# Optimization experiments

Measured on AMD Instinct MI355X. Metric: run time of the kernel, lower is better.

The kernel has to match this reference:

```python
import jax, jax.numpy as jnp
import numpy as np

B, T, F = 2048, 60, 89
H = 1024
OUT = 30  # output_predicted_chords


def setup_inputs() -> dict:
    key = jax.random.key(0)
    k1, k2, k3, k4 = jax.random.split(key, 4)
    # small init scale keeps the relu-activated recurrence numerically stable
    s = 0.02
    return {
        "x": jax.random.normal(k1, (B, T, F), dtype=jnp.float32),
        "W": jax.random.normal(k2, (F, 4 * H), dtype=jnp.float32) * s,
        "U": jax.random.normal(k3, (H, 4 * H), dtype=jnp.float32) * s,
        "b": jnp.zeros((4 * H,), dtype=jnp.float32),
        "Wd": jax.random.normal(k4, (H, OUT), dtype=jnp.float32) * s,
        "bd": jnp.zeros((OUT,), dtype=jnp.float32),
    }


def _lstm_last_h(x, W, U, b):
    """Keras LSTM(activation='relu', recurrent_activation='sigmoid').
    Gate order in Keras kernels: i, f, c (candidate), o.
    Returns last hidden state h_T of shape [B, H]."""
    Bsz = x.shape[0]
    Hdim = U.shape[0]
    # precompute input projections for all timesteps: [T, B, 4H]
    xz = jnp.einsum('btf,fg->tbg', x, W) + b

    def step(carry, xz_t):
        h, c = carry
        z = xz_t + h @ U                      # [B, 4H]
        i, f, g, o = jnp.split(z, 4, axis=-1)
        i = jax.nn.sigmoid(i)
        f = jax.nn.sigmoid(f)
        g = jax.nn.relu(g)                    # activation='relu' on candidate
        o = jax.nn.sigmoid(o)
        c = f * c + i * g
        h = o * jax.nn.relu(c)                # activation='relu' on cell output
        return (h, c), None

    h0 = jnp.zeros((Bsz, Hdim), dtype=x.dtype)
    c0 = jnp.zeros((Bsz, Hdim), dtype=x.dtype)
    (hT, _), _ = jax.lax.scan(step, (h0, c0), xz)
    return hT


def reference(x, W, U, b, Wd, bd):
    # LSTM(return_sequences=True) then take x[:, -1, :] == last hidden state
    hT = _lstm_last_h(x, W, U, b)             # [B, H]
    y = hT @ Wd + bd                           # [B, OUT]
    return y.reshape(-1, OUT, 1)               # [B, 30, 1]
```

## Files before the change

kernel.cpp:

```cpp
#include <hip/hip_runtime.h>
#include <cstdint>
#include <cstddef>

#define Bsz 2048
#define Tseq 60
#define Fin 89
#define Hd 1024
#define G4 4096
#define KX 96
#define NOUT 30

typedef _Float16 half8 __attribute__((ext_vector_type(8)));
typedef float f32x4 __attribute__((ext_vector_type(4)));

template <int N> struct IC { static constexpr int value = N; };

__device__ __forceinline__ void gload_lds16(const void* g, void* l) {
  __builtin_amdgcn_global_load_lds((const __attribute__((address_space(1))) void*)g,
                                   (__attribute__((address_space(3))) void*)l,
                                   16, 0, 0);
}

__device__ __forceinline__ float sigmoidf_fast(float x) {
  return 1.0f / (1.0f + __expf(-x));
}


__global__ __launch_bounds__(256) void convert_x(const float* __restrict__ x,
                                                 _Float16* __restrict__ xp) {
  int idx = blockIdx.x * 256 + threadIdx.x;
  int k = idx % KX;
  int b = (idx / KX) % Bsz;
  int t = idx / (KX * Bsz);
  float v = (k < Fin) ? x[((size_t)b * Tseq + t) * Fin + k] : 0.0f;
  xp[idx] = (_Float16)v;
}

__global__ __launch_bounds__(256) void transpose_W(const float* __restrict__ W,
                                                   _Float16* __restrict__ Wpt) {
  __shared__ float tile[32][33];
  int n0 = blockIdx.x * 32;
  int k0 = blockIdx.y * 32;
  int tx = threadIdx.x, ty = threadIdx.y;
  for (int i = ty; i < 32; i += 8) {
    int k = k0 + i;
    tile[i][tx] = (k < Fin) ? W[(size_t)k * G4 + n0 + tx] : 0.0f;
  }
  __syncthreads();
  for (int i = ty; i < 32; i += 8)
    Wpt[(size_t)(n0 + i) * KX + k0 + tx] = (_Float16)tile[tx][i];
}

__global__ __launch_bounds__(256) void transpose_U(const float* __restrict__ U,
                                                   _Float16* __restrict__ Upt) {
  __shared__ float tile[32][33];
  int n0 = blockIdx.x * 32;
  int k0 = blockIdx.y * 32;
  int tx = threadIdx.x, ty = threadIdx.y;
  for (int i = ty; i < 32; i += 8)
    tile[i][tx] = U[(size_t)(k0 + i) * G4 + n0 + tx];
  __syncthreads();
  for (int i = ty; i < 32; i += 8)
    Upt[(size_t)(n0 + i) * Hd + k0 + tx] = (_Float16)tile[tx][i];
}

__global__ __launch_bounds__(256, 2) void lstm_step(
    const _Float16* __restrict__ xp_t,
    const _Float16* __restrict__ Wpt,
    const _Float16* __restrict__ Upt,
    const float*    __restrict__ bias,
    const _Float16* __restrict__ h_in,
    _Float16*       __restrict__ h_out,
    float*          __restrict__ cst,
    int skip_h)
{
  __shared__ __align__(16) _Float16 As[3 * 4096];
  __shared__ __align__(16) _Float16 Bs[3 * 4096];

  const int tid  = threadIdx.x;
  const int wave = tid >> 6;
  const int lane = tid & 63;
  const int quad = lane >> 4;
  const int l16  = lane & 15;
  const int m0 = blockIdx.x * 128;
  const int j0 = blockIdx.y * 32;

  const int srow = lane >> 2;
  const int qg   = (lane & 3) ^ ((lane >> 3) & 3);
  const int sA   = quad ^ ((l16 >> 1) & 3);

  const int hb    = 16 * (wave & 1);
  const int mwave = 64 * (wave >> 1);
  const int j  = j0 + hb + l16;
  const int uA = 4 * (wave >> 1);
  const int uB = wave & 1;
  const int aoff = l16 * 32 + sA * 8;

  float bv[4];
  for (int p = 0; p < 4; ++p) bv[p] = bias[p * Hd + j];

  f32x4 acc[4][4];
  for (int mi = 0; mi < 4; ++mi)
    for (int p = 0; p < 4; ++p)
      acc[mi][p] = f32x4{bv[p], bv[p], bv[p], bv[p]};

  auto round = [&](auto ncI, const _Float16* __restrict__ Ab, int strA,
                   const _Float16* __restrict__ Bb, int strB, int k0) {
    constexpr int NC = decltype(ncI)::value;
    __syncthreads();
#pragma unroll
    for (int ii = 0; ii < NC * 2; ++ii) {
      int i = ii * 4 + wave;
      int st = i >> 3, ci = i & 7;
      gload_lds16(Ab + (size_t)(m0 + ci * 16 + srow) * strA + k0 + st * 32 + qg * 8,
                  &As[st * 4096 + ci * 512]);
    }
#pragma unroll
    for (int ii = 0; ii < NC * 2; ++ii) {
      int i = ii * 4 + wave;
      int st = i >> 3, ci = i & 7;
      int ln = ci * 16 + srow;
      int gn = (ln >> 5) * Hd + j0 + (ln & 31);
      gload_lds16(Bb + (size_t)gn * strB + k0 + st * 32 + qg * 8,
                  &Bs[st * 4096 + ci * 512]);
    }
    __syncthreads();
#pragma unroll
    for (int st = 0; st < NC; ++st) {
      half8 a[4], bq[4];
      for (int mi = 0; mi < 4; ++mi)
        a[mi] = *(const half8*)&As[st * 4096 + (uA + mi) * 512 + aoff];
      for (int p = 0; p < 4; ++p)
        bq[p] = *(const half8*)&Bs[st * 4096 + (2 * p + uB) * 512 + aoff];
      for (int mi = 0; mi < 4; ++mi)
        for (int p = 0; p < 4; ++p)
          acc[mi][p] = __builtin_amdgcn_mfma_f32_16x16x32_f16(a[mi], bq[p],
                                                              acc[mi][p],
                                                              0, 0, 0);
    }
  };

  round(IC<3>{}, xp_t, KX, Wpt, KX, 0);

  if (!skip_h) {
    for (int r = 0; r < 16; ++r)
      round(IC<2>{}, h_in, Hd, Upt, Hd, r * 64);
  }

  for (int mi = 0; mi < 4; ++mi) {
    for (int r = 0; r < 4; ++r) {
      int row = m0 + mwave + mi * 16 + quad * 4 + r;
      size_t idx = (size_t)row * Hd + j;
      float iv = sigmoidf_fast(acc[mi][0][r]);
      float fv = sigmoidf_fast(acc[mi][1][r]);
      float gv = fmaxf(acc[mi][2][r], 0.0f);
      float ov = sigmoidf_fast(acc[mi][3][r]);
      float cprev = skip_h ? 0.0f : cst[idx];
      float cv = fv * cprev + iv * gv;
      cst[idx] = cv;
      float hv = ov * fmaxf(cv, 0.0f);
      h_out[idx] = (_Float16)hv;
    }
  }
}

__global__ __launch_bounds__(256) void final_dense(const _Float16* __restrict__ h,
                                                   const float* __restrict__ Wd,
                                                   const float* __restrict__ bd,
                                                   float* __restrict__ y) {
  __shared__ float hs[Hd];
  __shared__ float red[8][32];
  int bi = blockIdx.x;
  for (int k = threadIdx.x; k < Hd; k += 256)
    hs[k] = (float)h[(size_t)bi * Hd + k];
  __syncthreads();
  int o  = threadIdx.x & 31;
  int ch = threadIdx.x >> 5;
  float p = 0.0f;
  if (o < NOUT) {
    int k0 = ch * (Hd / 8);
    for (int k = k0; k < k0 + (Hd / 8); ++k)
      p += hs[k] * Wd[(size_t)k * NOUT + o];
  }
  red[ch][o] = p;
  __syncthreads();
  if (threadIdx.x < NOUT) {
    float s = bd[threadIdx.x];
    for (int c2 = 0; c2 < 8; ++c2) s += red[c2][threadIdx.x];
    y[(size_t)bi * NOUT + threadIdx.x] = s;
  }
}


extern "C" void kernel_launch(void* const* d_in, const int* in_sizes, int n_in,
                              void* d_out, int out_size, void* d_ws, size_t ws_size,
                              hipStream_t stream) {
  const float* x  = (const float*)d_in[0];
  const float* W  = (const float*)d_in[1];
  const float* U  = (const float*)d_in[2];
  const float* b  = (const float*)d_in[3];
  const float* Wd = (const float*)d_in[4];
  const float* bd = (const float*)d_in[5];
  float* y = (float*)d_out;

  char* ws = (char*)d_ws;
  _Float16* xp  = (_Float16*)ws; ws += (size_t)Tseq * Bsz * KX * 2;
  _Float16* Wpt = (_Float16*)ws; ws += (size_t)G4 * KX * 2;
  _Float16* Upt = (_Float16*)ws; ws += (size_t)G4 * Hd * 2;
  _Float16* hb0 = (_Float16*)ws; ws += (size_t)Bsz * Hd * 2;
  _Float16* hb1 = (_Float16*)ws; ws += (size_t)Bsz * Hd * 2;
  float*    cst = (float*)ws;    ws += (size_t)Bsz * Hd * 4;

  convert_x<<<(Tseq * Bsz * KX) / 256, 256, 0, stream>>>(x, xp);
  transpose_W<<<dim3(G4 / 32, KX / 32), dim3(32, 8), 0, stream>>>(W, Wpt);
  transpose_U<<<dim3(G4 / 32, Hd / 32), dim3(32, 8), 0, stream>>>(U, Upt);

  for (int t = 0; t < Tseq; ++t) {
    const _Float16* hin  = ((t - 1) & 1) ? hb1 : hb0;
    _Float16*       hout = (t & 1) ? hb1 : hb0;
    lstm_step<<<dim3(Bsz / 128, G4 / 128), 256, 0, stream>>>(
        xp + (size_t)t * (Bsz * KX), Wpt, Upt, b,
        (t == 0) ? hb0 : hin, hout, cst, (t == 0) ? 1 : 0);
  }

  final_dense<<<Bsz, 256, 0, stream>>>(hb1, Wd, bd, y);
}
```

Measured before the change: 1.674 ms.

## Pre-swizzle weights into MFMA fragment layout and load B directly to registers

Weights W and U are packed once into a layout that matches the MFMA fragment order, so each wave reads its B operands straight from global/L2 into registers with double-buffered prefetch instead of staging them through LDS. The block tile shrinks to 128 rows by 16 hidden units with all four gates, the grid is reordered so blocks sharing a weight slice are launched together, and occupancy is raised to 4 blocks per CU. This removes LDS traffic and barriers for the weight operand, but each block now re-reads the h tile for a narrower slice of outputs and depends on L2 bandwidth for the B loads.

```diff
diff --git a/kernel.cpp b/kernel.cpp
--- a/kernel.cpp
+++ b/kernel.cpp
@@ -36,38 +36,36 @@
   xp[idx] = (_Float16)v;
 }
 
-__global__ __launch_bounds__(256) void transpose_W(const float* __restrict__ W,
-                                                   _Float16* __restrict__ Wpt) {
+__global__ __launch_bounds__(256) void pack_B(const float* __restrict__ src,
+                                              int kvalid, int ktbase,
+                                              _Float16* __restrict__ Bswz) {
   __shared__ float tile[32][33];
   int n0 = blockIdx.x * 32;
   int k0 = blockIdx.y * 32;
   int tx = threadIdx.x, ty = threadIdx.y;
   for (int i = ty; i < 32; i += 8) {
     int k = k0 + i;
-    tile[i][tx] = (k < Fin) ? W[(size_t)k * G4 + n0 + tx] : 0.0f;
+    tile[i][tx] = (k < kvalid) ? src[(size_t)k * G4 + n0 + tx] : 0.0f;
   }
   __syncthreads();
-  for (int i = ty; i < 32; i += 8)
-    Wpt[(size_t)(n0 + i) * KX + k0 + tx] = (_Float16)tile[tx][i];
-}
-
-__global__ __launch_bounds__(256) void transpose_U(const float* __restrict__ U,
-                                                   _Float16* __restrict__ Upt) {
-  __shared__ float tile[32][33];
-  int n0 = blockIdx.x * 32;
-  int k0 = blockIdx.y * 32;
-  int tx = threadIdx.x, ty = threadIdx.y;
-  for (int i = ty; i < 32; i += 8)
-    tile[i][tx] = U[(size_t)(k0 + i) * G4 + n0 + tx];
-  __syncthreads();
-  for (int i = ty; i < 32; i += 8)
-    Upt[(size_t)(n0 + i) * Hd + k0 + tx] = (_Float16)tile[tx][i];
-}
-
-__global__ __launch_bounds__(256, 2) void lstm_step(
+  int kt   = ktbase + (k0 >> 5);
+  int quad = (tx >> 3) & 3;
+  int e    = tx & 7;
+  for (int i = ty; i < 32; i += 8) {
+    int n = n0 + i;
+    int p = n >> 10;
+    int jj = n & 1023;
+    int jb = jj >> 4;
+    int l16 = jj & 15;
+    int lane = quad * 16 + l16;
+    size_t dst = ((size_t)(jb * 35 + kt) * 4 + p) * 512 + lane * 8 + e;
+    Bswz[dst] = (_Float16)tile[tx][i];
+  }
+}
+
+__global__ __launch_bounds__(256, 4) void lstm_step(
     const _Float16* __restrict__ xp_t,
-    const _Float16* __restrict__ Wpt,
-    const _Float16* __restrict__ Upt,
+    const _Float16* __restrict__ Bswz,
     const float*    __restrict__ bias,
     const _Float16* __restrict__ h_in,
     _Float16*       __restrict__ h_out,
@@ -75,81 +73,106 @@
     int skip_h)
 {
   __shared__ __align__(16) _Float16 As[3 * 4096];
-  __shared__ __align__(16) _Float16 Bs[3 * 4096];
 
   const int tid  = threadIdx.x;
   const int wave = tid >> 6;
   const int lane = tid & 63;
   const int quad = lane >> 4;
   const int l16  = lane & 15;
-  const int m0 = blockIdx.x * 128;
-  const int j0 = blockIdx.y * 32;
+  const int jb = blockIdx.x;
+  const int m0 = blockIdx.y * 128;
+  const int j0 = jb * 16;
 
   const int srow = lane >> 2;
   const int qg   = (lane & 3) ^ ((lane >> 3) & 3);
   const int sA   = quad ^ ((l16 >> 1) & 3);
-
-  const int hb    = 16 * (wave & 1);
-  const int mwave = 64 * (wave >> 1);
-  const int j  = j0 + hb + l16;
-  const int uA = 4 * (wave >> 1);
-  const int uB = wave & 1;
+  const int j    = j0 + l16;
   const int aoff = l16 * 32 + sA * 8;
+  const int uA   = wave * 2;
+
+  const _Float16* Bb = Bswz + (size_t)jb * (35 * 2048) + lane * 8;
 
   float bv[4];
+#pragma unroll
   for (int p = 0; p < 4; ++p) bv[p] = bias[p * Hd + j];
 
-  f32x4 acc[4][4];
-  for (int mi = 0; mi < 4; ++mi)
+  f32x4 acc[2][4];
+#pragma unroll
+  for (int mi = 0; mi < 2; ++mi)
+#pragma unroll
     for (int p = 0; p < 4; ++p)
       acc[mi][p] = f32x4{bv[p], bv[p], bv[p], bv[p]};
 
-  auto round = [&](auto ncI, const _Float16* __restrict__ Ab, int strA,
-                   const _Float16* __restrict__ Bb, int strB, int k0) {
+  const int ktmax = skip_h ? 2 : 34;
+
+  half8 bq0[4], bq1[4];
+#pragma unroll
+  for (int p = 0; p < 4; ++p) bq0[p] = *(const half8*)(Bb + p * 512);
+
+  auto stage = [&](auto ncI, const _Float16* __restrict__ Ab, int strA,
+                   int k0g) {
     constexpr int NC = decltype(ncI)::value;
     __syncthreads();
 #pragma unroll
     for (int ii = 0; ii < NC * 2; ++ii) {
       int i = ii * 4 + wave;
       int st = i >> 3, ci = i & 7;
-      gload_lds16(Ab + (size_t)(m0 + ci * 16 + srow) * strA + k0 + st * 32 + qg * 8,
+      gload_lds16(Ab + (size_t)(m0 + ci * 16 + srow) * strA + k0g + st * 32 + qg * 8,
                   &As[st * 4096 + ci * 512]);
     }
-#pragma unroll
-    for (int ii = 0; ii < NC * 2; ++ii) {
-      int i = ii * 4 + wave;
-      int st = i >> 3, ci = i & 7;
-      int ln = ci * 16 + srow;
-      int gn = (ln >> 5) * Hd + j0 + (ln & 31);
-      gload_lds16(Bb + (size_t)gn * strB + k0 + st * 32 + qg * 8,
-                  &Bs[st * 4096 + ci * 512]);
-    }
     __syncthreads();
-#pragma unroll
-    for (int st = 0; st < NC; ++st) {
-      half8 a[4], bq[4];
-      for (int mi = 0; mi < 4; ++mi)
-        a[mi] = *(const half8*)&As[st * 4096 + (uA + mi) * 512 + aoff];
-      for (int p = 0; p < 4; ++p)
-        bq[p] = *(const half8*)&Bs[st * 4096 + (2 * p + uB) * 512 + aoff];
-      for (int mi = 0; mi < 4; ++mi)
-        for (int p = 0; p < 4; ++p)
-          acc[mi][p] = __builtin_amdgcn_mfma_f32_16x16x32_f16(a[mi], bq[p],
-                                                              acc[mi][p],
-                                                              0, 0, 0);
-    }
   };
 
-  round(IC<3>{}, xp_t, KX, Wpt, KX, 0);
+  auto sub = [&](auto parI, int ktg, int stl) {
+    constexpr int P = decltype(parI)::value;
+    int ktn = (ktg < ktmax) ? ktg + 1 : ktg;
+    const _Float16* bp = Bb + (size_t)ktn * 2048;
+    if constexpr (P == 0) {
+#pragma unroll
+      for (int p = 0; p < 4; ++p) bq1[p] = *(const half8*)(bp + p * 512);
+    } else {
+#pragma unroll
+      for (int p = 0; p < 4; ++p) bq0[p] = *(const half8*)(bp + p * 512);
+    }
+    half8 a0 = *(const half8*)&As[stl * 4096 + uA * 512 + aoff];
+    half8 a1 = *(const half8*)&As[stl * 4096 + (uA + 1) * 512 + aoff];
+    if constexpr (P == 0) {
+#pragma unroll
+      for (int p = 0; p < 4; ++p) {
+        acc[0][p] = __builtin_amdgcn_mfma_f32_16x16x32_f16(a0, bq0[p],
+                                                           acc[0][p], 0, 0, 0);
+        acc[1][p] = __builtin_amdgcn_mfma_f32_16x16x32_f16(a1, bq0[p],
+                                                           acc[1][p], 0, 0, 0);
+      }
+    } else {
+#pragma unroll
+      for (int p = 0; p < 4; ++p) {
+        acc[0][p] = __builtin_amdgcn_mfma_f32_16x16x32_f16(a0, bq1[p],
+                                                           acc[0][p], 0, 0, 0);
+        acc[1][p] = __builtin_amdgcn_mfma_f32_16x16x32_f16(a1, bq1[p],
+                                                           acc[1][p], 0, 0, 0);
+      }
+    }
+  };
+
+  stage(IC<3>{}, xp_t, KX, 0);
+  sub(IC<0>{}, 0, 0);
+  sub(IC<1>{}, 1, 1);
+  sub(IC<0>{}, 2, 2);
 
   if (!skip_h) {
-    for (int r = 0; r < 16; ++r)
-      round(IC<2>{}, h_in, Hd, Upt, Hd, r * 64);
-  }
-
-  for (int mi = 0; mi < 4; ++mi) {
+    for (int r = 0; r < 16; ++r) {
+      stage(IC<2>{}, h_in, Hd, r * 64);
+      sub(IC<1>{}, 3 + 2 * r, 0);
+      sub(IC<0>{}, 4 + 2 * r, 1);
+    }
+  }
+
+#pragma unroll
+  for (int mi = 0; mi < 2; ++mi) {
+#pragma unroll
     for (int r = 0; r < 4; ++r) {
-      int row = m0 + mwave + mi * 16 + quad * 4 + r;
+      int row = m0 + wave * 32 + mi * 16 + quad * 4 + r;
       size_t idx = (size_t)row * Hd + j;
       float iv = sigmoidf_fast(acc[mi][0][r]);
       float fv = sigmoidf_fast(acc[mi][1][r]);
@@ -204,22 +227,21 @@
   float* y = (float*)d_out;
 
   char* ws = (char*)d_ws;
-  _Float16* xp  = (_Float16*)ws; ws += (size_t)Tseq * Bsz * KX * 2;
-  _Float16* Wpt = (_Float16*)ws; ws += (size_t)G4 * KX * 2;
-  _Float16* Upt = (_Float16*)ws; ws += (size_t)G4 * Hd * 2;
-  _Float16* hb0 = (_Float16*)ws; ws += (size_t)Bsz * Hd * 2;
-  _Float16* hb1 = (_Float16*)ws; ws += (size_t)Bsz * Hd * 2;
-  float*    cst = (float*)ws;    ws += (size_t)Bsz * Hd * 4;
+  _Float16* xp   = (_Float16*)ws; ws += (size_t)Tseq * Bsz * KX * 2;
+  _Float16* Bswz = (_Float16*)ws; ws += (size_t)64 * 35 * 2048 * 2;
+  _Float16* hb0  = (_Float16*)ws; ws += (size_t)Bsz * Hd * 2;
+  _Float16* hb1  = (_Float16*)ws; ws += (size_t)Bsz * Hd * 2;
+  float*    cst  = (float*)ws;    ws += (size_t)Bsz * Hd * 4;
 
   convert_x<<<(Tseq * Bsz * KX) / 256, 256, 0, stream>>>(x, xp);
-  transpose_W<<<dim3(G4 / 32, KX / 32), dim3(32, 8), 0, stream>>>(W, Wpt);
-  transpose_U<<<dim3(G4 / 32, Hd / 32), dim3(32, 8), 0, stream>>>(U, Upt);
+  pack_B<<<dim3(G4 / 32, 3),       dim3(32, 8), 0, stream>>>(W, Fin, 0, Bswz);
+  pack_B<<<dim3(G4 / 32, Hd / 32), dim3(32, 8), 0, stream>>>(U, Hd,  3, Bswz);
 
   for (int t = 0; t < Tseq; ++t) {
     const _Float16* hin  = ((t - 1) & 1) ? hb1 : hb0;
     _Float16*       hout = (t & 1) ? hb1 : hb0;
-    lstm_step<<<dim3(Bsz / 128, G4 / 128), 256, 0, stream>>>(
-        xp + (size_t)t * (Bsz * KX), Wpt, Upt, b,
+    lstm_step<<<dim3(64, 16), 256, 0, stream>>>(
+        xp + (size_t)t * (Bsz * KX), Bswz, b,
         (t == 0) ? hb0 : hin, hout, cst, (t == 0) ? 1 : 0);
   }
 
```

Measured after the change: 2.358 ms. 40.9% more time.

## Fuse LSTM timesteps into one persistent kernel with grid barriers

Applied to the files above, without the earlier changes.

Replaces the 60 per-timestep kernel launches with a single persistent kernel of 512 blocks that loops over time and synchronises through an atomic-counter grid barrier. The cell state now stays in registers instead of being read from and written to global memory every step. The input projection for step t is issued before the barrier, so it overlaps with blocks that are still finishing the previous step. The design relies on all 512 blocks being co-resident (2 per CU). The barrier has a spin guard that can break out early, which could silently produce wrong results if it ever fires.

```diff
diff --git a/kernel.cpp b/kernel.cpp
--- a/kernel.cpp
+++ b/kernel.cpp
@@ -9,6 +9,7 @@
 #define G4 4096
 #define KX 96
 #define NOUT 30
+#define NBLK 512
 
 typedef _Float16 half8 __attribute__((ext_vector_type(8)));
 typedef float f32x4 __attribute__((ext_vector_type(4)));
@@ -25,6 +26,27 @@
   return 1.0f / (1.0f + __expf(-x));
 }
 
+__device__ __forceinline__ void grid_barrier(unsigned int* bar,
+                                             unsigned int target) {
+  __builtin_amdgcn_s_waitcnt(0);
+  __syncthreads();
+  if (threadIdx.x == 0) {
+    __hip_atomic_fetch_add(bar, 1u, __ATOMIC_RELEASE, __HIP_MEMORY_SCOPE_AGENT);
+    unsigned int guard = 0;
+    while (__hip_atomic_load(bar, __ATOMIC_RELAXED,
+                             __HIP_MEMORY_SCOPE_AGENT) < target) {
+      __builtin_amdgcn_s_sleep(2);
+      if (++guard > (1u << 20)) break;
+    }
+    (void)__hip_atomic_load(bar, __ATOMIC_ACQUIRE, __HIP_MEMORY_SCOPE_AGENT);
+  }
+  __syncthreads();
+}
+
+
+__global__ __launch_bounds__(64) void zero_bar(unsigned int* bar) {
+  if (threadIdx.x == 0) *bar = 0u;
+}
 
 __global__ __launch_bounds__(256) void convert_x(const float* __restrict__ x,
                                                  _Float16* __restrict__ xp) {
@@ -64,15 +86,14 @@
     Upt[(size_t)(n0 + i) * Hd + k0 + tx] = (_Float16)tile[tx][i];
 }
 
-__global__ __launch_bounds__(256, 2) void lstm_step(
-    const _Float16* __restrict__ xp_t,
+__global__ __launch_bounds__(256, 2) void lstm_persist(
+    const _Float16* __restrict__ xp,
     const _Float16* __restrict__ Wpt,
     const _Float16* __restrict__ Upt,
     const float*    __restrict__ bias,
-    const _Float16* __restrict__ h_in,
-    _Float16*       __restrict__ h_out,
-    float*          __restrict__ cst,
-    int skip_h)
+    _Float16*       __restrict__ hb0,
+    _Float16*       __restrict__ hb1,
+    unsigned int*   __restrict__ bar)
 {
   __shared__ __align__(16) _Float16 As[3 * 4096];
   __shared__ __align__(16) _Float16 Bs[3 * 4096];
@@ -97,12 +118,16 @@
   const int aoff = l16 * 32 + sA * 8;
 
   float bv[4];
+#pragma unroll
   for (int p = 0; p < 4; ++p) bv[p] = bias[p * Hd + j];
 
+  float cr[4][4];
+#pragma unroll
+  for (int mi = 0; mi < 4; ++mi)
+#pragma unroll
+    for (int r = 0; r < 4; ++r) cr[mi][r] = 0.0f;
+
   f32x4 acc[4][4];
-  for (int mi = 0; mi < 4; ++mi)
-    for (int p = 0; p < 4; ++p)
-      acc[mi][p] = f32x4{bv[p], bv[p], bv[p], bv[p]};
 
   auto round = [&](auto ncI, const _Float16* __restrict__ Ab, int strA,
                    const _Float16* __restrict__ Bb, int strB, int k0) {
@@ -140,26 +165,37 @@
     }
   };
 
-  round(IC<3>{}, xp_t, KX, Wpt, KX, 0);
-
-  if (!skip_h) {
-    for (int r = 0; r < 16; ++r)
-      round(IC<2>{}, h_in, Hd, Upt, Hd, r * 64);
-  }
-
-  for (int mi = 0; mi < 4; ++mi) {
-    for (int r = 0; r < 4; ++r) {
-      int row = m0 + mwave + mi * 16 + quad * 4 + r;
-      size_t idx = (size_t)row * Hd + j;
-      float iv = sigmoidf_fast(acc[mi][0][r]);
-      float fv = sigmoidf_fast(acc[mi][1][r]);
-      float gv = fmaxf(acc[mi][2][r], 0.0f);
-      float ov = sigmoidf_fast(acc[mi][3][r]);
-      float cprev = skip_h ? 0.0f : cst[idx];
-      float cv = fv * cprev + iv * gv;
-      cst[idx] = cv;
-      float hv = ov * fmaxf(cv, 0.0f);
-      h_out[idx] = (_Float16)hv;
+  for (int t = 0; t < Tseq; ++t) {
+#pragma unroll
+    for (int mi = 0; mi < 4; ++mi)
+#pragma unroll
+      for (int p = 0; p < 4; ++p)
+        acc[mi][p] = f32x4{bv[p], bv[p], bv[p], bv[p]};
+
+    round(IC<3>{}, xp + (size_t)t * (Bsz * KX), KX, Wpt, KX, 0);
+
+    if (t > 0) {
+      grid_barrier(bar, (unsigned int)t * NBLK);
+      const _Float16* hprev = ((t - 1) & 1) ? hb1 : hb0;
+      for (int r = 0; r < 16; ++r)
+        round(IC<2>{}, hprev, Hd, Upt, Hd, r * 64);
+    }
+
+    _Float16* hout = (t & 1) ? hb1 : hb0;
+#pragma unroll
+    for (int mi = 0; mi < 4; ++mi) {
+#pragma unroll
+      for (int r = 0; r < 4; ++r) {
+        int row = m0 + mwave + mi * 16 + quad * 4 + r;
+        float iv = sigmoidf_fast(acc[mi][0][r]);
+        float fv = sigmoidf_fast(acc[mi][1][r]);
+        float gv = fmaxf(acc[mi][2][r], 0.0f);
+        float ov = sigmoidf_fast(acc[mi][3][r]);
+        float cv = fv * cr[mi][r] + iv * gv;
+        cr[mi][r] = cv;
+        float hv = ov * fmaxf(cv, 0.0f);
+        hout[(size_t)row * Hd + j] = (_Float16)hv;
+      }
     }
   }
 }
@@ -209,19 +245,15 @@
   _Float16* Upt = (_Float16*)ws; ws += (size_t)G4 * Hd * 2;
   _Float16* hb0 = (_Float16*)ws; ws += (size_t)Bsz * Hd * 2;
   _Float16* hb1 = (_Float16*)ws; ws += (size_t)Bsz * Hd * 2;
-  float*    cst = (float*)ws;    ws += (size_t)Bsz * Hd * 4;
-
+  unsigned int* bar = (unsigned int*)ws; ws += 256;
+
+  zero_bar<<<1, 64, 0, stream>>>(bar);
   convert_x<<<(Tseq * Bsz * KX) / 256, 256, 0, stream>>>(x, xp);
   transpose_W<<<dim3(G4 / 32, KX / 32), dim3(32, 8), 0, stream>>>(W, Wpt);
   transpose_U<<<dim3(G4 / 32, Hd / 32), dim3(32, 8), 0, stream>>>(U, Upt);
 
-  for (int t = 0; t < Tseq; ++t) {
-    const _Float16* hin  = ((t - 1) & 1) ? hb1 : hb0;
-    _Float16*       hout = (t & 1) ? hb1 : hb0;
-    lstm_step<<<dim3(Bsz / 128, G4 / 128), 256, 0, stream>>>(
-        xp + (size_t)t * (Bsz * KX), Wpt, Upt, b,
-        (t == 0) ? hb0 : hin, hout, cst, (t == 0) ? 1 : 0);
-  }
+  lstm_persist<<<dim3(Bsz / 128, G4 / 128), 256, 0, stream>>>(
+      xp, Wpt, Upt, b, hb0, hb1, bar);
 
   final_dense<<<Bsz, 256, 0, stream>>>(hb1, Wd, bd, y);
 }
```

Result: slower. 2.678 ms (+59.9%).
